# Kernel tuning notes

Hardware: AMD Instinct MI355X
Metric: run time of the kernel (lower is better)

The kernel has to match this reference:

```python
import jax, jax.numpy as jnp
import numpy as np

EPS = 1e-5
NUM_CRYSTALS = 64


def _bn(x2d, g, b):
    # torch BatchNorm1d in training mode: biased batch stats, affine
    m = x2d.mean(0)
    v = x2d.var(0)
    return g * (x2d - m) * jax.lax.rsqrt(v + EPS) + b


def _improved_conv(x, e, idx, p):
    (fcW, fcb, g1, b1, g2, b2, eW, eb, ge, be, W3, b3, g3, b3b) = p
    N, M = idx.shape
    A = x.shape[1]
    Bf = e.shape[2]
    xn = x[idx]  # (N, M, A) gathered neighbor atom features
    tot = jnp.concatenate([jnp.broadcast_to(x[:, None, :], (N, M, A)), xn, e], axis=2)  # (N,M,2A+B)
    # 2-body gated message
    h = jnp.einsum('nmf,of->nmo', tot, fcW) + fcb
    h = _bn(h.reshape(-1, 2 * A), g1, b1).reshape(N, M, 2 * A)
    two_body = jnp.sum(jax.nn.sigmoid(h[..., :A]) * jax.nn.softplus(h[..., A:]), axis=1)
    # explicit edge update
    he = jnp.einsum('nmf,of->nmo', tot, eW) + eb
    he = _bn(he.reshape(-1, 2 * Bf), ge, be).reshape(N, M, 2 * Bf)
    e_out = e + jax.nn.sigmoid(he[..., :Bf]) * jax.nn.softplus(he[..., Bf:])
    # 3-body: split W3 by concat blocks [x_i, x_j, x_l, e_ij, e_il] so the
    # (N,M,M,3A+2B) concat is never materialized; only (N,M,M,2A) is formed.
    Wa, Wj, Wl, Wij, Wil = jnp.split(W3, [A, 2 * A, 3 * A, 3 * A + Bf], axis=1)
    h3 = ((x @ Wa.T)[:, None, None, :]
          + (xn @ Wj.T)[:, :, None, :]
          + (xn @ Wl.T)[:, None, :, :]
          + (e @ Wij.T)[:, :, None, :]
          + (e @ Wil.T)[:, None, :, :]
          + b3)  # (N, M, M, 2A)
    h3 = _bn(h3.reshape(-1, 2 * A), g3, b3b).reshape(N, M, M, 2 * A)
    three_body = jnp.sum(jax.nn.sigmoid(h3[..., :A]) * jax.nn.softplus(h3[..., A:]), axis=(1, 2))
    total = _bn(two_body + three_body, g2, b2)
    return jax.nn.softplus(x + total), e_out


def setup_inputs() -> dict:
    key = jax.random.key(0)
    ks = jax.random.split(key, 12)
    N, M, OF, A, BF, H, NC = 2000, 12, 92, 64, 41, 128, 3
    f = lambda k, s: jax.random.normal(k, s, dtype=jnp.float32) * 0.05
    z = lambda s: jnp.zeros(s, jnp.float32)
    o = lambda s: jnp.ones(s, jnp.float32)
    return {
        'atom_fea': jax.random.normal(ks[0], (N, OF), dtype=jnp.float32),
        'nbr_fea': jax.random.normal(ks[1], (N, M, BF), dtype=jnp.float32),
        'nbr_fea_idx': jax.random.randint(ks[2], (N, M), 0, N),
        'site_seg': jnp.sort(jax.random.randint(ks[3], (N,), 0, NUM_CRYSTALS)),
        'emb_W': f(ks[4], (A, OF)), 'emb_b': z((A,)),
        'fcW': f(ks[5], (NC, 2 * A, 2 * A + BF)), 'fcb': z((NC, 2 * A)),
        'bn1_g': o((NC, 2 * A)), 'bn1_b': z((NC, 2 * A)),
        'bn2_g': o((NC, A)), 'bn2_b': z((NC, A)),
        'eW': f(ks[6], (NC, 2 * BF, 2 * A + BF)), 'eb': z((NC, 2 * BF)),
        'bne_g': o((NC, 2 * BF)), 'bne_b': z((NC, 2 * BF)),
        'W3': f(ks[7], (NC, 2 * A, 3 * A + 2 * BF)), 'b3': z((NC, 2 * A)),
        'bn3_g': o((NC, 2 * A)), 'bn3_b': z((NC, 2 * A)),
        'fc1W': f(ks[8], (H, A)), 'fc1b': z((H,)),
        'outW': f(ks[9], (1, H)), 'outb': z((1,)),
    }


def reference(atom_fea, nbr_fea, nbr_fea_idx, site_seg, emb_W, emb_b,
              fcW, fcb, bn1_g, bn1_b, bn2_g, bn2_b, eW, eb, bne_g, bne_b,
              W3, b3, bn3_g, bn3_b, fc1W, fc1b, outW, outb):
    x = atom_fea @ emb_W.T + emb_b  # embedding1 (orbital=False)
    e = nbr_fea
    n_conv = fcW.shape[0]
    for i in range(n_conv):  # small fixed layer loop
        p = (fcW[i], fcb[i], bn1_g[i], bn1_b[i], bn2_g[i], bn2_b[i],
             eW[i], eb[i], bne_g[i], bne_b[i], W3[i], b3[i], bn3_g[i], bn3_b[i])
        x, e = _improved_conv(x, e, nbr_fea_idx, p)
    x = jax.nn.softplus(jax.nn.softplus(x) @ fc1W.T + fc1b)  # conv_to_fc1
    # per-crystal mean pooling over site segments
    N = x.shape[0]
    sums = jax.ops.segment_sum(x, site_seg, num_segments=NUM_CRYSTALS)
    counts = jax.ops.segment_sum(jnp.ones((N, 1), x.dtype), site_seg, num_segments=NUM_CRYSTALS)
    pooled = sums / jnp.maximum(counts, 1.0)
    return pooled @ outW.T + outb  # (NUM_CRYSTALS, 1)
```

## Files before the change

kernel.cpp:

```cpp
#include <hip/hip_runtime.h>
#include <hip/hip_bf16.h>

#define N_ATOM 2000
#define MNBR   12
#define OFEA   92
#define AF     64
#define BFEA   41
#define K1     169
#define O1     128
#define OE     82
#define NM     24000
#define NCONV  3
#define HID    128
#define NCRY   64
#define EPS_BN 1e-5f

#define LDA_T  192
#define LDH    512
#define LDSW   88
#define LDE    48

typedef __bf16 bf16x8 __attribute__((ext_vector_type(8)));
typedef float  f32x4  __attribute__((ext_vector_type(4)));

__device__ __forceinline__ float sigmoidf_(float x){
    return __builtin_amdgcn_rcpf(1.f + __expf(-x));
}
__device__ __forceinline__ float softplusf_(float x){
    return fmaxf(x,0.f) + __logf(1.f + __expf(-fabsf(x)));
}

__global__ __launch_bounds__(256, 3)
void gemm_fused(const unsigned short* __restrict__ Xb,
                const unsigned short* __restrict__ E48b,
                const int*   __restrict__ idx,
                const __hip_bfloat16* __restrict__ W,
                const float* __restrict__ bias,
                float* __restrict__ REST,
                float* __restrict__ STL,
                float* __restrict__ SPA,
                float* __restrict__ SQA)
{
    __shared__ unsigned short As[128][LDSW];
    __shared__ unsigned short Ws[128][LDSW];
    __shared__ float cs1[128];
    __shared__ float cs2[128];
    __shared__ float spa[12][128];

    const int tid  = threadIdx.x;
    const int row0 = blockIdx.x * 128;
    const int col0 = blockIdx.y * 128;
    const int w    = tid >> 6;
    const int l    = tid & 63;
    const int wm   = w >> 1, wn = w & 1;
    const int lrow = l & 15;
    const int quad = l >> 4;

    if (tid < 128){ cs1[tid] = 0.f; cs2[tid] = 0.f; }
    for (int ii = tid; ii < 12*128; ii += 256) spa[ii>>7][ii&127] = 0.f;

    f32x4 acc[4][4];
    #pragma unroll
    for (int i=0;i<4;i++)
        #pragma unroll
        for (int j=0;j<4;j++) acc[i][j] = (f32x4){0.f,0.f,0.f,0.f};

    #pragma unroll
    for (int it = 0; it < 3; ++it){
        const int k0 = it * 64;
        if (it) __syncthreads();
        #pragma unroll
        for (int j = 0; j < 4; ++j){
            int e   = tid + j*256;
            int r   = e >> 3;
            int kk8 = (e & 7);
            int grow = row0 + r;
            uint4 va = make_uint4(0,0,0,0);
            if (grow < NM){
                if (it == 2){
                    if (kk8 < 6)
                        va = *(const uint4*)(E48b + (size_t)grow*LDE + kk8*8);
                } else {
                    const unsigned short* s = (it == 0)
                        ? Xb + (size_t)((unsigned)grow/12u)*AF + kk8*8
                        : Xb + (size_t)idx[grow]*AF + kk8*8;
                    va = *(const uint4*)s;
                }
            }
            *(uint4*)(&As[r][kk8*8]) = va;
            uint4 vw = *(const uint4*)(W + (size_t)(col0 + r)*LDA_T + k0 + kk8*8);
            *(uint4*)(&Ws[r][kk8*8]) = vw;
        }
        __syncthreads();
        #pragma unroll
        for (int ks = 0; ks < 2; ++ks){
            int koff = ks*32 + quad*8;
            bf16x8 a_[4], b_[4];
            #pragma unroll
            for (int mi=0;mi<4;mi++)
                a_[mi] = *(const bf16x8*)(&As[wm*64 + mi*16 + lrow][koff]);
            #pragma unroll
            for (int ni=0;ni<4;ni++)
                b_[ni] = *(const bf16x8*)(&Ws[wn*64 + ni*16 + lrow][koff]);
            #pragma unroll
            for (int mi=0;mi<4;mi++)
                #pragma unroll
                for (int ni=0;ni<4;ni++)
                    acc[mi][ni] = __builtin_amdgcn_mfma_f32_16x16x32_bf16(
                        a_[mi], b_[ni], acc[mi][ni], 0, 0, 0);
        }
    }

    const bool isPQ = (col0 >= 256);
    const int atomBase = (unsigned)row0 / 12u;
    int rbase_[4], n0_[4], sp_[4];
    #pragma unroll
    for (int mi=0;mi<4;mi++){
        rbase_[mi] = row0 + wm*64 + mi*16 + quad*4;
        int n0 = (int)((unsigned)rbase_[mi] / 12u);
        n0_[mi] = n0;
        sp_[mi] = 12 - (rbase_[mi] - n0*12);
    }

    #pragma unroll
    for (int ni=0;ni<4;ni++){
        const int cl  = wn*64 + ni*16 + lrow;
        const int col = col0 + cl;
        const float bv = bias[col];
        float s1 = 0.f, s2 = 0.f;
        #pragma unroll
        for (int mi=0;mi<4;mi++){
            const int rbase = rbase_[mi];
            float run0 = 0.f, run1 = 0.f;
            #pragma unroll
            for (int reg=0;reg<4;reg++){
                int grow = rbase + reg;
                if (grow < NM){
                    float vv = acc[mi][ni][reg] + bv;
                    if (col0 != 128 || col < 210)
                        REST[(size_t)grow*LDH + col] = vv;
                    s1 += vv; s2 += vv*vv;
                    if (isPQ){
                        if (reg < sp_[mi]) run0 += vv; else run1 += vv;
                    }
                }
            }
            if (isPQ){
                if (run0 != 0.f) atomicAdd(&spa[n0_[mi]     - atomBase][cl], run0);
                if (run1 != 0.f) atomicAdd(&spa[n0_[mi] + 1 - atomBase][cl], run1);
            }
        }
        if (isPQ){
            atomicAdd(&cs2[cl], s2);
        } else {
            atomicAdd(&cs1[cl], s1);
            atomicAdd(&cs2[cl], s2);
        }
    }
    __syncthreads();
    if (!isPQ){
        if (tid < 128){
            atomicAdd(&STL[col0 + tid],       cs1[tid]);
            atomicAdd(&STL[256 + col0 + tid], cs2[tid]);
        }
    } else {
        if (tid < 128)
            atomicAdd(&STL[(col0 == 256 ? 896 : 1024) + tid], cs2[tid]);
        float* SPQd = (col0 == 256) ? SPA : SQA;
        for (int ii = tid; ii < 12*128; ii += 256){
            int ai = ii >> 7, c2 = ii & 127;
            int na = atomBase + ai;
            float val = spa[ai][c2];
            if (val != 0.f && na < N_ATOM)
                atomicAdd(&SPQd[(size_t)na*128 + c2], val);
        }
    }
}

__global__ __launch_bounds__(256)
void bn3_pre(const float* __restrict__ SPA, const float* __restrict__ SQA,
             float* __restrict__ STL)
{
    const int c    = threadIdx.x & 127;
    const int half = threadIdx.x >> 7;
    float s1 = 0.f, sx = 0.f;
    for (int n = blockIdx.x*2 + half; n < N_ATOM; n += 250){
        float p = SPA[(size_t)n*128 + c];
        float q = SQA[(size_t)n*128 + c];
        s1 += p + q;
        sx += p * q;
    }
    atomicAdd(&STL[512 + c], 12.f*s1);
    atomicAdd(&STL[640 + c], 2.f*sx);
}

__global__ __launch_bounds__(256)
void emb_k(const float* __restrict__ A, const float* __restrict__ Wm,
           const float* __restrict__ b, float* __restrict__ X,
           __hip_bfloat16* __restrict__ Xb)
{
    __shared__ float Ws[64][93];
    __shared__ float As[16][93];
    const int t = threadIdx.x;
    const int n0 = blockIdx.x * 16;
    for (int i = t; i < 64*OFEA; i += 256){
        int c = i / OFEA, k = i % OFEA;
        Ws[c][k] = Wm[i];
    }
    for (int i = t; i < 16*OFEA; i += 256){
        int r = i / OFEA, k = i % OFEA;
        As[r][k] = A[(size_t)(n0 + r)*OFEA + k];
    }
    __syncthreads();
    const int r  = t >> 4;
    const int c0 = (t & 15) * 4;
    float a0=0.f, a1=0.f, a2=0.f, a3=0.f;
    for (int k = 0; k < OFEA; ++k){
        float av = As[r][k];
        a0 += av * Ws[c0+0][k];
        a1 += av * Ws[c0+1][k];
        a2 += av * Ws[c0+2][k];
        a3 += av * Ws[c0+3][k];
    }
    size_t o = (size_t)(n0 + r)*AF + c0;
    float v0 = a0 + b[c0+0], v1 = a1 + b[c0+1];
    float v2 = a2 + b[c0+2], v3 = a3 + b[c0+3];
    X[o+0] = v0; X[o+1] = v1; X[o+2] = v2; X[o+3] = v3;
    Xb[o+0] = __float2bfloat16(v0); Xb[o+1] = __float2bfloat16(v1);
    Xb[o+2] = __float2bfloat16(v2); Xb[o+3] = __float2bfloat16(v3);
}

__global__ __launch_bounds__(256)
void head_k(const float* __restrict__ X, const float* __restrict__ Wm,
            const float* __restrict__ b, float* __restrict__ Z)
{
    __shared__ float Ws[128][65];
    __shared__ float Xs[16][65];
    const int t = threadIdx.x;
    const int n0 = blockIdx.x * 16;
    for (int i = t; i < 128*AF; i += 256){
        int c = i >> 6, k = i & 63;
        Ws[c][k] = Wm[i];
    }
    for (int i = t; i < 16*AF; i += 256){
        int r = i >> 6, k = i & 63;
        Xs[r][k] = softplusf_(X[(size_t)(n0 + r)*AF + k]);
    }
    __syncthreads();
    const int r  = t >> 4;
    const int c0 = (t & 15) * 8;
    float acc[8];
    #pragma unroll
    for (int j=0;j<8;j++) acc[j] = 0.f;
    for (int k = 0; k < AF; ++k){
        float xv = Xs[r][k];
        #pragma unroll
        for (int j=0;j<8;j++)
            acc[j] += xv * Ws[c0+j][k];
    }
    size_t o = (size_t)(n0 + r)*HID + c0;
    #pragma unroll
    for (int j=0;j<8;j++)
        Z[o+j] = softplusf_(acc[j] + b[c0+j]);
}

__global__ void prologue_k(const float* __restrict__ fcW, const float* __restrict__ eW,
                           const float* __restrict__ W3, const float* __restrict__ fcb,
                           const float* __restrict__ eb, const float* __restrict__ b3,
                           const float* __restrict__ nbr,
                           __hip_bfloat16* __restrict__ WALL, float* __restrict__ BIAS,
                           float* __restrict__ E48, __hip_bfloat16* __restrict__ E48b,
                           float* __restrict__ ZR)
{
    int i = blockIdx.x*blockDim.x + threadIdx.x;
    const int nW = NCONV*512*LDA_T;
    const int nB = NCONV*512;
    const int nE = NM*LDE;
    if (i < nW){
        int ll = i/(512*LDA_T), rem = i%(512*LDA_T);
        int c = rem/LDA_T, k = rem%LDA_T;
        float v = 0.f;
        if (c < O1){
            if (k < K1) v = fcW[((size_t)ll*O1 + c)*K1 + k];
        } else if (c < O1+OE){
            if (k < K1) v = eW[((size_t)ll*OE + (c-O1))*K1 + k];
        } else if (c >= 256 && c < 384){
            int o = c - 256;
            const float* W3l = W3 + (size_t)ll*O1*274;
            if (k < AF)                        v = 0.5f * W3l[(size_t)o*274 + k];
            else if (k < 2*AF)                 v = W3l[(size_t)o*274 + k];
            else if (k < K1)                   v = W3l[(size_t)o*274 + 192 + (k-128)];
        } else if (c >= 384){
            int o = c - 384;
            const float* W3l = W3 + (size_t)ll*O1*274;
            if (k < AF)                        v = 0.5f * W3l[(size_t)o*274 + k];
            else if (k < 2*AF)                 v = W3l[(size_t)o*274 + k + AF];
            else if (k < K1)                   v = W3l[(size_t)o*274 + 233 + (k-128)];
        }
        WALL[i] = __float2bfloat16(v);
    } else if (i < nW + nB){
        int m = i - nW;
        int ll = m/512, c = m%512;
        float v = 0.f;
        if (c < O1)         v = fcb[ll*O1 + c];
        else if (c < O1+OE) v = eb[ll*OE + (c-O1)];
        else if (c >= 256)  v = 0.5f * b3[ll*O1 + ((c-256)&127)];
        BIAS[m] = v;
    } else if (i < nW + nB + nE){
        int j = i - (nW + nB);
        int r = j / LDE, k = j % LDE;
        float v = (k < BFEA) ? nbr[(size_t)r*BFEA + k] : 0.f;
        E48[j]  = v;
        E48b[j] = __float2bfloat16(v);
    } else {
        int j = i - (nW + nB + nE);
        ZR[j] = 0.f;
    }
}

__global__ __launch_bounds__(256)
void consumer_k(const float* __restrict__ REST, const float* __restrict__ STL,
                float* __restrict__ TB, float* __restrict__ E48,
                __hip_bfloat16* __restrict__ E48b,
                const float* __restrict__ g1, const float* __restrict__ b1,
                const float* __restrict__ ge, const float* __restrict__ be,
                const float* __restrict__ g3, const float* __restrict__ b3b)
{
    __shared__ float red[256];
    __shared__ float scA[210], shA[210], sc3v[128], sh3v[128];
    const int n = blockIdx.x;
    const int t = threadIdx.x;
    const int a = t & 63;
    const int g = t >> 6;

    if (t < 210){
        float mean = STL[t]*(1.f/NM);
        float var  = fmaxf(STL[256+t]*(1.f/NM) - mean*mean, 0.f);
        float gg = (t < O1) ? g1[t] : ge[t-O1];
        float bb = (t < O1) ? b1[t] : be[t-O1];
        float sc = gg * rsqrtf(var + EPS_BN);
        scA[t] = sc; shA[t] = bb - sc*mean;
    }
    if (t < 128){
        float inv  = 1.f/((float)NM*MNBR);
        float mean = STL[512+t]*inv;
        float ex2  = (STL[640+t] + 12.f*(STL[896+t] + STL[1024+t]))*inv;
        float var  = fmaxf(ex2 - mean*mean, 0.f);
        float sc = g3[t] * rsqrtf(var + EPS_BN);
        sc3v[t] = sc; sh3v[t] = b3b[t] - sc*mean;
    }
    __syncthreads();

    const float* base = REST + (size_t)n*MNBR*LDH;
    const float s3lo = sc3v[a],  s3hi = sc3v[64+a];
    const float t3lo = sh3v[a],  t3hi = sh3v[64+a];

    float Ea[MNBR], Fb[MNBR];
    #pragma unroll
    for (int m=0;m<MNBR;m++){
        const float* row = base + (size_t)m*LDH;
        Ea[m] = __expf(-(s3lo*row[384+a]));
        Fb[m] = __expf( (s3hi*row[448+a]));
    }
    const float sha = scA[a],    tha = shA[a];
    const float shb = scA[64+a], thb = shA[64+a];
    float acc = 0.f;
    #pragma unroll
    for (int j=0;j<3;j++){
        const float* row = base + (size_t)(g*3+j)*LDH;
        acc += sigmoidf_(sha*row[a]+tha) * softplusf_(shb*row[64+a]+thb);
        float ua = s3lo*row[256+a] + t3lo;
        float ub = s3hi*row[320+a] + t3hi;
        float Em = __expf(-ua);
        float Fm = __expf(ub);
        #pragma unroll
        for (int l2=0;l2<MNBR;l2++){
            float s = __builtin_amdgcn_rcpf(1.f + Em*Ea[l2]);
            float p = __logf(1.f + Fm*Fb[l2]);
            acc += s*p;
        }
    }
    red[t] = acc;
    __syncthreads();
    if (t < 64)
        TB[(size_t)n*AF + t] = red[t] + red[64+t] + red[128+t] + red[192+t];
    for (int idx = t; idx < MNBR*BFEA; idx += 256){
        int m = idx / BFEA, b = idx % BFEA;
        const float* row = base + (size_t)m*LDH;
        float u = scA[O1+b]*row[O1+b]   + shA[O1+b];
        float v = scA[169+b]*row[169+b] + shA[169+b];
        size_t eo = ((size_t)n*MNBR + m)*LDE + b;
        float nv = E48[eo] + sigmoidf_(u) * softplusf_(v);
        E48[eo]  = nv;
        E48b[eo] = __float2bfloat16(nv);
    }
}

__global__ __launch_bounds__(256)
void xupd_k(float* __restrict__ X, __hip_bfloat16* __restrict__ Xb,
            const float* __restrict__ TB, float* __restrict__ STL,
            const float* __restrict__ g2, const float* __restrict__ b2)
{
    __shared__ float r1[256], r2[256];
    const int t = threadIdx.x;
    const int a = t & 63, rg = t >> 6;
    float s1 = 0.f, s2 = 0.f;
    for (int r = blockIdx.x*4 + rg; r < N_ATOM; r += 256){
        float v = TB[(size_t)r*AF + a];
        s1 += v; s2 += v*v;
    }
    r1[t] = s1; r2[t] = s2;
    __syncthreads();
    if (t < 64){
        s1 = r1[t]+r1[64+t]+r1[128+t]+r1[192+t];
        s2 = r2[t]+r2[64+t]+r2[128+t]+r2[192+t];
        atomicAdd(&STL[768+t], s1);
        atomicAdd(&STL[832+t], s2);
    }
    __syncthreads();
    if (t == 0){
        unsigned* cnt = (unsigned*)&STL[1200];
        __hip_atomic_fetch_add(cnt, 1u, __ATOMIC_ACQ_REL, __HIP_MEMORY_SCOPE_AGENT);
        while (__hip_atomic_load(cnt, __ATOMIC_ACQUIRE, __HIP_MEMORY_SCOPE_AGENT) < 64u)
            __builtin_amdgcn_s_sleep(2);
    }
    __syncthreads();
    float sA = __hip_atomic_load(&STL[768+a], __ATOMIC_RELAXED, __HIP_MEMORY_SCOPE_AGENT);
    float sB = __hip_atomic_load(&STL[832+a], __ATOMIC_RELAXED, __HIP_MEMORY_SCOPE_AGENT);
    float mean = sA*(1.f/N_ATOM);
    float var  = fmaxf(sB*(1.f/N_ATOM) - mean*mean, 0.f);
    float sc = g2[a]*rsqrtf(var + EPS_BN);
    float sh = b2[a] - sc*mean;
    for (int i = blockIdx.x*256 + t; i < N_ATOM*AF; i += 64*256){
        float v = softplusf_(X[i] + sc*TB[i] + sh);
        X[i]  = v;
        Xb[i] = __float2bfloat16(v);
    }
}

__global__ __launch_bounds__(128)
void pool_out_k(const float* __restrict__ Z, const int* __restrict__ seg,
                const float* __restrict__ outW, const float* __restrict__ outb,
                float* __restrict__ out)
{
    __shared__ float red[128];
    const int c = blockIdx.x;
    const int h = threadIdx.x;
    int l0, l1;
    {
        int l=0, r=N_ATOM;
        while (l<r){ int m=(l+r)>>1; if (seg[m] < c) l=m+1; else r=m; }
        l0 = l;
        l=l0; r=N_ATOM;
        while (l<r){ int m=(l+r)>>1; if (seg[m] < c+1) l=m+1; else r=m; }
        l1 = l;
    }
    float s = 0.f;
    for (int n = l0; n < l1; ++n) s += Z[(size_t)n*HID + h];
    float cnt = fmaxf((float)(l1-l0), 1.f);
    red[h] = (s/cnt) * outW[h];
    __syncthreads();
    for (int off=64; off>0; off>>=1){
        if (h < off) red[h] += red[h+off];
        __syncthreads();
    }
    if (h == 0) out[c] = red[0] + outb[0];
}

extern "C" void kernel_launch(void* const* d_in, const int* in_sizes, int n_in,
                              void* d_out, int out_size, void* d_ws, size_t ws_size,
                              hipStream_t stream)
{
    const float* atom_fea = (const float*)d_in[0];
    const float* nbr_fea  = (const float*)d_in[1];
    const int*   nbr_idx  = (const int*)d_in[2];
    const int*   site_seg = (const int*)d_in[3];
    const float* emb_W = (const float*)d_in[4];
    const float* emb_b = (const float*)d_in[5];
    const float* fcW   = (const float*)d_in[6];
    const float* fcb   = (const float*)d_in[7];
    const float* bn1_g = (const float*)d_in[8];
    const float* bn1_b = (const float*)d_in[9];
    const float* bn2_g = (const float*)d_in[10];
    const float* bn2_b = (const float*)d_in[11];
    const float* eW    = (const float*)d_in[12];
    const float* eb    = (const float*)d_in[13];
    const float* bne_g = (const float*)d_in[14];
    const float* bne_b = (const float*)d_in[15];
    const float* W3    = (const float*)d_in[16];
    const float* b3    = (const float*)d_in[17];
    const float* bn3_g = (const float*)d_in[18];
    const float* bn3_b = (const float*)d_in[19];
    const float* fc1W  = (const float*)d_in[20];
    const float* fc1b  = (const float*)d_in[21];
    const float* outW  = (const float*)d_in[22];
    const float* outb  = (const float*)d_in[23];

    float* ws   = (float*)d_ws;
    float* X    = ws;
    float* E48  = ws + 128000;
    float* REST = ws + 1280000;
    float* TB   = ws + 13568000;
    float* Z    = ws + 13696000;
    float* ST   = ws + 13952000;
    float* SPQ  = ws + 13959168;
    __hip_bfloat16* WALL = (__hip_bfloat16*)(ws + 15495168);
    float* BIAS = ws + 15642624;
    __hip_bfloat16* Xb   = (__hip_bfloat16*)(ws + 15644160);
    __hip_bfloat16* E48b = (__hip_bfloat16*)(ws + 15708160);

    {
        const int total = 294912 + 1536 + 1152000 + 1543168;
        prologue_k<<<total/256, 256, 0, stream>>>(fcW, eW, W3, fcb, eb, b3, nbr_fea,
                                                  WALL, BIAS, E48, E48b, ST);
    }
    emb_k<<<N_ATOM/16, 256, 0, stream>>>(atom_fea, emb_W, emb_b, X, Xb);

    for (int i = 0; i < NCONV; i++){
        float* STL = ST + i*2048;
        float* SPA = SPQ + (size_t)i*512000;
        float* SQA = SPA + 256000;

        {
            dim3 g((NM+127)/128, 4);
            gemm_fused<<<g, 256, 0, stream>>>((const unsigned short*)Xb,
                                              (const unsigned short*)E48b, nbr_idx,
                                              WALL + (size_t)i*512*LDA_T,
                                              BIAS + i*512, REST, STL, SPA, SQA);
        }
        bn3_pre<<<125, 256, 0, stream>>>(SPA, SQA, STL);
        consumer_k<<<N_ATOM, 256, 0, stream>>>(REST, STL, TB, E48, E48b,
                                               bn1_g + i*O1, bn1_b + i*O1,
                                               bne_g + i*OE, bne_b + i*OE,
                                               bn3_g + i*O1, bn3_b + i*O1);
        xupd_k<<<64, 256, 0, stream>>>(X, Xb, TB, STL,
                                       bn2_g + i*AF, bn2_b + i*AF);
    }

    head_k<<<N_ATOM/16, 256, 0, stream>>>(X, fc1W, fc1b, Z);
    pool_out_k<<<NCRY, 128, 0, stream>>>(Z, site_seg, outW, outb, (float*)d_out);
}
```

Measured before the change: 353.1 us.

## Stage GEMM epilogue through LDS for coalesced stores and serial column reductions

The GEMM epilogue now writes accumulator tiles (plus bias) into an LDS buffer that reuses the A/W staging memory, two 64-row halves at a time. Rows are then written to global memory with float4 stores instead of scattered scalar stores. Column sums, sums of squares and per-atom segment sums are computed by a serial per-column scan in place of shared-memory atomics. A second, separate change hoists all global loads in the three-body kernel ahead of the transcendental math so more loads are in flight. Costs: extra barriers, and the column scan runs on only 128 threads over 64 rows.

```diff
diff --git a/kernel.cpp b/kernel.cpp
--- a/kernel.cpp
+++ b/kernel.cpp
@@ -19,6 +19,7 @@
 #define LDH    512
 #define LDSW   88
 #define LDE    48
+#define LDD    132
 
 typedef __bf16 bf16x8 __attribute__((ext_vector_type(8)));
 typedef float  f32x4  __attribute__((ext_vector_type(4)));
@@ -41,10 +42,10 @@
                 float* __restrict__ SPA,
                 float* __restrict__ SQA)
 {
-    __shared__ unsigned short As[128][LDSW];
-    __shared__ unsigned short Ws[128][LDSW];
-    __shared__ float cs1[128];
-    __shared__ float cs2[128];
+    __shared__ __align__(16) char smem_u[45056];
+    unsigned short (*As)[LDSW] = (unsigned short(*)[LDSW])smem_u;
+    unsigned short (*Ws)[LDSW] = (unsigned short(*)[LDSW])(smem_u + 22528);
+    float (*dump)[LDD] = (float(*)[LDD])smem_u;
     __shared__ float spa[12][128];
 
     const int tid  = threadIdx.x;
@@ -56,7 +57,6 @@
     const int lrow = l & 15;
     const int quad = l >> 4;
 
-    if (tid < 128){ cs1[tid] = 0.f; cs2[tid] = 0.f; }
     for (int ii = tid; ii < 12*128; ii += 256) spa[ii>>7][ii&127] = 0.f;
 
     f32x4 acc[4][4];
@@ -111,61 +111,70 @@
         }
     }
 
-    const bool isPQ = (col0 >= 256);
-    const int atomBase = (unsigned)row0 / 12u;
-    int rbase_[4], n0_[4], sp_[4];
-    #pragma unroll
-    for (int mi=0;mi<4;mi++){
-        rbase_[mi] = row0 + wm*64 + mi*16 + quad*4;
-        int n0 = (int)((unsigned)rbase_[mi] / 12u);
-        n0_[mi] = n0;
-        sp_[mi] = 12 - (rbase_[mi] - n0*12);
-    }
-
-    #pragma unroll
-    for (int ni=0;ni<4;ni++){
-        const int cl  = wn*64 + ni*16 + lrow;
-        const int col = col0 + cl;
-        const float bv = bias[col];
-        float s1 = 0.f, s2 = 0.f;
-        #pragma unroll
-        for (int mi=0;mi<4;mi++){
-            const int rbase = rbase_[mi];
-            float run0 = 0.f, run1 = 0.f;
+    const bool isPQ  = (col0 >= 256);
+    const int  rem12 = row0 % 12;
+    float s1 = 0.f, s2 = 0.f;
+
+    #pragma unroll
+    for (int p = 0; p < 2; ++p){
+        __syncthreads();
+        if (wm == p){
             #pragma unroll
-            for (int reg=0;reg<4;reg++){
-                int grow = rbase + reg;
-                if (grow < NM){
-                    float vv = acc[mi][ni][reg] + bv;
-                    if (col0 != 128 || col < 210)
-                        REST[(size_t)grow*LDH + col] = vv;
-                    s1 += vv; s2 += vv*vv;
-                    if (isPQ){
-                        if (reg < sp_[mi]) run0 += vv; else run1 += vv;
-                    }
+            for (int mi=0;mi<4;mi++){
+                #pragma unroll
+                for (int ni=0;ni<4;ni++){
+                    int lr = mi*16 + quad*4;
+                    int cl = wn*64 + ni*16 + lrow;
+                    float bv = bias[col0 + cl];
+                    dump[lr+0][cl] = acc[mi][ni][0] + bv;
+                    dump[lr+1][cl] = acc[mi][ni][1] + bv;
+                    dump[lr+2][cl] = acc[mi][ni][2] + bv;
+                    dump[lr+3][cl] = acc[mi][ni][3] + bv;
                 }
             }
-            if (isPQ){
-                if (run0 != 0.f) atomicAdd(&spa[n0_[mi]     - atomBase][cl], run0);
-                if (run1 != 0.f) atomicAdd(&spa[n0_[mi] + 1 - atomBase][cl], run1);
+        }
+        __syncthreads();
+        {
+            int lr  = tid >> 2;
+            int cs0 = (tid & 3) * 32;
+            int grow = row0 + p*64 + lr;
+            if (grow < NM){
+                float* dst = REST + (size_t)grow*LDH + col0 + cs0;
+                const float* srcr = dump[lr] + cs0;
+                #pragma unroll
+                for (int c8=0;c8<8;c8++)
+                    *(float4*)(dst + c8*4) = *(const float4*)(srcr + c8*4);
             }
         }
-        if (isPQ){
-            atomicAdd(&cs2[cl], s2);
-        } else {
-            atomicAdd(&cs1[cl], s1);
-            atomicAdd(&cs2[cl], s2);
+        if (tid < 128){
+            const int c  = tid;
+            const int x0 = p*64;
+            float run = 0.f;
+            int aiPrev = (rem12 + x0) / 12;
+            for (int r = 0; r < 64; ++r){
+                int grow = row0 + x0 + r;
+                if (grow >= NM) break;
+                float v = dump[r][c];
+                s1 += v; s2 += v*v;
+                if (isPQ){
+                    int ai = (rem12 + x0 + r) / 12;
+                    if (ai != aiPrev){ spa[aiPrev][c] += run; run = 0.f; aiPrev = ai; }
+                    run += v;
+                }
+            }
+            if (isPQ && run != 0.f) spa[aiPrev][c] += run;
         }
     }
     __syncthreads();
     if (!isPQ){
         if (tid < 128){
-            atomicAdd(&STL[col0 + tid],       cs1[tid]);
-            atomicAdd(&STL[256 + col0 + tid], cs2[tid]);
+            atomicAdd(&STL[col0 + tid],       s1);
+            atomicAdd(&STL[256 + col0 + tid], s2);
         }
     } else {
         if (tid < 128)
-            atomicAdd(&STL[(col0 == 256 ? 896 : 1024) + tid], cs2[tid]);
+            atomicAdd(&STL[(col0 == 256 ? 896 : 1024) + tid], s2);
+        const int atomBase = row0 / 12;
         float* SPQd = (col0 == 256) ? SPA : SQA;
         for (int ii = tid; ii < 12*128; ii += 256){
             int ai = ii >> 7, c2 = ii & 127;
@@ -352,25 +361,39 @@
     __syncthreads();
 
     const float* base = REST + (size_t)n*MNBR*LDH;
+
+    float vQa[MNBR], vQb[MNBR];
+    #pragma unroll
+    for (int m=0;m<MNBR;m++){
+        vQa[m] = base[(size_t)m*LDH + 384 + a];
+        vQb[m] = base[(size_t)m*LDH + 448 + a];
+    }
+    float vh[3], vk[3], vP[3], vV[3];
+    #pragma unroll
+    for (int j=0;j<3;j++){
+        const float* row = base + (size_t)(g*3+j)*LDH;
+        vh[j] = row[a];
+        vk[j] = row[64+a];
+        vP[j] = row[256+a];
+        vV[j] = row[320+a];
+    }
+
     const float s3lo = sc3v[a],  s3hi = sc3v[64+a];
     const float t3lo = sh3v[a],  t3hi = sh3v[64+a];
-
     float Ea[MNBR], Fb[MNBR];
     #pragma unroll
     for (int m=0;m<MNBR;m++){
-        const float* row = base + (size_t)m*LDH;
-        Ea[m] = __expf(-(s3lo*row[384+a]));
-        Fb[m] = __expf( (s3hi*row[448+a]));
+        Ea[m] = __expf(-(s3lo*vQa[m]));
+        Fb[m] = __expf( (s3hi*vQb[m]));
     }
     const float sha = scA[a],    tha = shA[a];
     const float shb = scA[64+a], thb = shA[64+a];
     float acc = 0.f;
     #pragma unroll
     for (int j=0;j<3;j++){
-        const float* row = base + (size_t)(g*3+j)*LDH;
-        acc += sigmoidf_(sha*row[a]+tha) * softplusf_(shb*row[64+a]+thb);
-        float ua = s3lo*row[256+a] + t3lo;
-        float ub = s3hi*row[320+a] + t3hi;
+        acc += sigmoidf_(sha*vh[j]+tha) * softplusf_(shb*vk[j]+thb);
+        float ua = s3lo*vP[j] + t3lo;
+        float ub = s3hi*vV[j] + t3hi;
         float Em = __expf(-ua);
         float Fm = __expf(ub);
         #pragma unroll
```

Result: slower. 363.2 us (+2.9%).
